# Kernel tuning notes

Measured on AMD Instinct MI355X. Metric: run time of the kernel, lower is better.

Reference implementation:

```python
import jax, jax.numpy as jnp
import numpy as np


def setup_inputs() -> dict:
    key = jax.random.key(0)
    ks = jax.random.split(key, 8)
    T, B, O, H, A = 512, 256, 720, 128, 2
    s = lambda k, shp, sc: (jax.random.normal(k, shp, jnp.float32) * sc)
    return {
        "x": jax.random.normal(ks[0], (T, B, O), jnp.float32),
        "h0": jnp.zeros((B, H), jnp.float32),
        "c0": jnp.zeros((B, H), jnp.float32),
        "Wx": s(ks[1], (O, 4 * H), 1.0 / np.sqrt(O)),
        "Wh": s(ks[2], (H, 4 * H), 1.0 / np.sqrt(H)),
        "b": jnp.zeros((4 * H,), jnp.float32),
        "Wa1": s(ks[3], (H, H), np.sqrt(2.0 / H)),
        "ba1": jnp.zeros((H,), jnp.float32),
        "Wa2": s(ks[4], (H, A), 0.01),
        "ba2": jnp.zeros((A,), jnp.float32),
        "log_std": jnp.zeros((A,), jnp.float32),
        "Wc1": s(ks[5], (H, H), np.sqrt(2.0 / H)),
        "bc1": jnp.zeros((H,), jnp.float32),
        "Wc2": s(ks[6], (H, 1), 0.01),
        "bc2": jnp.zeros((1,), jnp.float32),
    }


def _lstm(x, h0, c0, Wx, Wh, b):
    # Precompute input projections for all timesteps: [T, B, 4H]
    xW = jnp.einsum('tbo,og->tbg', x, Wx) + b

    def step(carry, xw_t):
        h, c = carry
        gates = xw_t + h @ Wh  # [B, 4H]
        i, f, g, o = jnp.split(gates, 4, axis=-1)
        c = jax.nn.sigmoid(f) * c + jax.nn.sigmoid(i) * jnp.tanh(g)
        h = jax.nn.sigmoid(o) * jnp.tanh(c)
        return (h, c), h

    (hT, cT), _ = jax.lax.scan(step, (h0, c0), xW)
    return hT, cT


def reference(x, h0, c0, Wx, Wh, b, Wa1, ba1, Wa2, ba2, log_std,
              Wc1, bc1, Wc2, bc2):
    hT, cT = _lstm(x, h0, c0, Wx, Wh, b)
    feat = hT  # outputs[-1] == last hidden state (unidirectional)
    actor_mean = jnp.tanh(feat @ Wa1 + ba1) @ Wa2 + ba2  # [B, A]
    std = jnp.exp(log_std)  # [A]
    value = (jnp.tanh(feat @ Wc1 + bc1) @ Wc2 + bc2).squeeze(-1)  # [B]
    return actor_mean, std, value, hT, cT
```

## Files before the change

### kernel.cpp

```cpp
#include <hip/hip_runtime.h>
#include <hip/hip_bf16.h>

typedef unsigned int   u32;
typedef unsigned short u16;
typedef _Float16       f16;
typedef __attribute__((ext_vector_type(2))) _Float16 f16x2;
typedef __attribute__((ext_vector_type(8))) _Float16 f16x8;
typedef __attribute__((ext_vector_type(4))) float    f32x4;
typedef __attribute__((ext_vector_type(4))) u32      u32x4;

#define T_STEPS 512
#define BATCH   256
#define O_IN    720
#define KPAD    736
#define HID     128
#define G4      512
#define OUT_STD 512
#define OUT_VAL 514
#define OUT_HT  770
#define OUT_CT  33538

static const unsigned long long XW_OFF  = 0ull;
static const unsigned long long WXT_OFF = 134217728ull;

__device__ inline float exp2raw(float x){
  float r; asm("v_exp_f32 %0, %1" : "=v"(r) : "v"(x)); return r;
}
__device__ inline float rcpraw(float x){
  float r; asm("v_rcp_f32 %0, %1" : "=v"(r) : "v"(x)); return r;
}
__device__ inline float sigf(float x){ return rcpraw(1.0f + exp2raw(-1.44269504f * x)); }
__device__ inline float tanhfast(float x){
  return fmaf(2.f, rcpraw(1.0f + exp2raw(-2.88539008f * x)), -1.f);
}

__device__ inline float dot2f(u32 a, u32 b, float c){
  float d;
  asm("v_dot2_f32_f16 %0, %1, %2, %3" : "=v"(d) : "v"(a), "v"(b), "v"(c));
  return d;
}

#define DPPF(x, ctrl) \
  __uint_as_float((u32)__builtin_amdgcn_update_dpp(0, (int)__float_as_uint(x), (ctrl), 0xF, 0xF, false))

#define HQ_STRIDE 80
#define H_BYTES   (4*HQ_STRIDE)
#define HW_OFF(j) (((j)>>5)*HQ_STRIDE + ((j)&31)*2)

__global__ void k_pack_wxt(const float* __restrict__ Wx, u16* __restrict__ wxt){
  const int n = blockIdx.x;
  for (int k = threadIdx.x; k < KPAD; k += 256){
    float v = (k < O_IN) ? Wx[(size_t)k * G4 + n] : 0.f;
    wxt[(size_t)n * KPAD + k] = __builtin_bit_cast(u16, (f16)v);
  }
}

__global__ __launch_bounds__(256, 2) void k_gemm(const float* __restrict__ x,
                                                 const u16* __restrict__ wxt,
                                                 u16* __restrict__ xw)
{
  const int l  = threadIdx.x & 63;
  const int w  = threadIdx.x >> 6;
  const int lr = l & 15;
  const int lk = l >> 4;
  const u32 L  = (blockIdx.x & 7u) * 256u + (blockIdx.x >> 3);
  const u32 mb = L >> 2, nb = L & 3u;
  const u32 M0 = mb * 256u + (u32)w * 64u;
  const u32 N0 = nb * 128u;

  const float* ax[4];
  const u16*   bx[8];
#pragma unroll
  for (int mf = 0; mf < 4; ++mf)
    ax[mf] = x + (unsigned long long)(M0 + mf*16 + lr) * O_IN + lk*8;
#pragma unroll
  for (int nf = 0; nf < 8; ++nf)
    bx[nf] = wxt + (unsigned long long)(N0 + nf*16 + lr) * KPAD + lk*8;

  f32x4 acc[4][8];
#pragma unroll
  for (int mf = 0; mf < 4; ++mf)
#pragma unroll
    for (int nf = 0; nf < 8; ++nf)
      acc[mf][nf] = (f32x4){0.f, 0.f, 0.f, 0.f};

  f32x4 a0[4][2];
  f16x8 aF[4], bF[8];

#pragma unroll
  for (int mf = 0; mf < 4; ++mf){
    a0[mf][0] = *(const f32x4*)(ax[mf]);
    a0[mf][1] = *(const f32x4*)(ax[mf] + 4);
  }
#pragma unroll
  for (int nf = 0; nf < 8; ++nf)
    bF[nf] = *(const f16x8*)(bx[nf]);
#pragma unroll
  for (int mf = 0; mf < 4; ++mf){
    f32x4 lo = a0[mf][0], hi = a0[mf][1];
    f16x8 v; v[0]=(f16)lo.x; v[1]=(f16)lo.y; v[2]=(f16)lo.z; v[3]=(f16)lo.w;
             v[4]=(f16)hi.x; v[5]=(f16)hi.y; v[6]=(f16)hi.z; v[7]=(f16)hi.w;
    aF[mf] = v;
  }

  for (int kc = 0; kc < 22; ++kc){
    if (kc < 21){
#pragma unroll
      for (int mf = 0; mf < 4; ++mf){
        a0[mf][0] = *(const f32x4*)(ax[mf] + (kc+1)*32);
        a0[mf][1] = *(const f32x4*)(ax[mf] + (kc+1)*32 + 4);
      }
    }
#pragma unroll
    for (int nf = 0; nf < 8; ++nf){
#pragma unroll
      for (int mf = 0; mf < 4; ++mf)
        acc[mf][nf] = __builtin_amdgcn_mfma_f32_16x16x32_f16(aF[mf], bF[nf], acc[mf][nf], 0, 0, 0);
      if (kc < 21)
        bF[nf] = *(const f16x8*)(bx[nf] + (kc+1)*32);
    }
    if (kc < 21){
#pragma unroll
      for (int mf = 0; mf < 4; ++mf){
        f32x4 lo = a0[mf][0], hi = a0[mf][1];
        f16x8 v; v[0]=(f16)lo.x; v[1]=(f16)lo.y; v[2]=(f16)lo.z; v[3]=(f16)lo.w;
                 v[4]=(f16)hi.x; v[5]=(f16)hi.y; v[6]=(f16)hi.z; v[7]=(f16)hi.w;
        aF[mf] = v;
      }
    }
  }

  {
    f16x8 aT[4];
#pragma unroll
    for (int mf = 0; mf < 4; ++mf) aT[mf] = (f16x8)(f16)0.f;
    if (lk < 2){
#pragma unroll
      for (int mf = 0; mf < 4; ++mf){
        f32x4 lo = *(const f32x4*)(ax[mf] + 704);
        f32x4 hi = *(const f32x4*)(ax[mf] + 708);
        f16x8 v; v[0]=(f16)lo.x; v[1]=(f16)lo.y; v[2]=(f16)lo.z; v[3]=(f16)lo.w;
                 v[4]=(f16)hi.x; v[5]=(f16)hi.y; v[6]=(f16)hi.z; v[7]=(f16)hi.w;
        aT[mf] = v;
      }
    }
#pragma unroll
    for (int nf = 0; nf < 8; ++nf){
      f16x8 bT = *(const f16x8*)(bx[nf] + 704);
#pragma unroll
      for (int mf = 0; mf < 4; ++mf)
        acc[mf][nf] = __builtin_amdgcn_mfma_f32_16x16x32_f16(aT[mf], bT, acc[mf][nf], 0, 0, 0);
    }
  }

#pragma unroll
  for (int mf = 0; mf < 4; ++mf){
    const u32 rowb = M0 + mf*16 + lk*4;
#pragma unroll
    for (int nf = 0; nf < 8; ++nf){
      const u32 col = N0 + nf*16 + lr;
#pragma unroll
      for (int r = 0; r < 4; ++r)
        xw[(unsigned long long)(rowb + r) * G4 + col] = __builtin_bit_cast(u16, (f16)acc[mf][nf][r]);
    }
  }
}

__global__ __attribute__((amdgpu_flat_work_group_size(512,512), amdgpu_waves_per_eu(2,2)))
void k_rnn(
    const u16* __restrict__ xw, const float* __restrict__ Wh,
    const float* __restrict__ h0, const float* __restrict__ c0,
    const float* __restrict__ bvec,
    const float* __restrict__ Wa1, const float* __restrict__ ba1,
    const float* __restrict__ Wa2, const float* __restrict__ ba2,
    const float* __restrict__ Wc1, const float* __restrict__ bc1,
    const float* __restrict__ Wc2, const float* __restrict__ bc2,
    const float* __restrict__ log_std, float* __restrict__ out)
{
  const int b = blockIdx.x;
  const int t = threadIdx.x;
  const int j = t >> 2;
  const int q = t & 3;

  __shared__ __align__(16) char hbuf[2][H_BYTES];
  __shared__ __align__(16) float hf[HID];
  __shared__ float hid[256];

  u32 wg0[16], wg1[16], wg2[16], wg3[16];
#pragma unroll
  for (int m = 0; m < 16; ++m){
    const u32 kb = (u32)(32*q + 2*m) * G4 + (u32)j;
    f16x2 p;
    p[0]=(f16)Wh[kb      ]; p[1]=(f16)Wh[kb+G4      ]; wg0[m]=__builtin_bit_cast(u32,p);
    p[0]=(f16)Wh[kb+128  ]; p[1]=(f16)Wh[kb+G4+128  ]; wg1[m]=__builtin_bit_cast(u32,p);
    p[0]=(f16)Wh[kb+256  ]; p[1]=(f16)Wh[kb+G4+256  ]; wg2[m]=__builtin_bit_cast(u32,p);
    p[0]=(f16)Wh[kb+384  ]; p[1]=(f16)Wh[kb+G4+384  ]; wg3[m]=__builtin_bit_cast(u32,p);
  }
#pragma unroll
  for (int m = 0; m < 16; ++m){
    asm volatile("" : "+v"(wg0[m]));
    asm volatile("" : "+v"(wg1[m]));
    asm volatile("" : "+v"(wg2[m]));
    asm volatile("" : "+v"(wg3[m]));
  }
  const float bb = bvec[j + 128*q];

  const float kexp  = (q == 2) ? -2.88539008f : -1.44269504f;
  const float postm = (q == 2) ? 2.f : 1.f;
  const float posta = (q == 2) ? -1.f : 0.f;

  float cs = c0[b*HID + j];
  float hv = h0[b*HID + j];
  if (q == 0)
    *(u16*)(hbuf[0] + HW_OFF(j)) = __builtin_bit_cast(u16, (f16)hv);
  __syncthreads();

  const u16* xp = xw + (u32)b * G4 + (u32)(j + 128*q);
  float xc  = (float)__builtin_bit_cast(f16, xp[0]) + bb;
  float xn1 = (T_STEPS > 1) ? (float)__builtin_bit_cast(f16, xp[131072u]) + bb : 0.f;

  for (int s = 0; s < T_STEPS; ++s){
    const char* hq = hbuf[s & 1] + q * HQ_STRIDE;

    float xn2 = 0.f;
    if (s + 2 < T_STEPS)
      xn2 = (float)__builtin_bit_cast(f16, xp[(u32)(s+2) * 131072u]) + bb;

    float p0 = 0.f, p1 = 0.f, p2 = 0.f, p3 = 0.f;
#pragma unroll
    for (int it = 0; it < 4; ++it){
      u32x4 hh = *(const u32x4*)(hq + it*16);
#pragma unroll
      for (int z = 0; z < 4; ++z){
        p0 = dot2f(hh[z], wg0[4*it+z], p0);
        p1 = dot2f(hh[z], wg1[4*it+z], p1);
        p2 = dot2f(hh[z], wg2[4*it+z], p2);
        p3 = dot2f(hh[z], wg3[4*it+z], p3);
      }
    }
    p0 += DPPF(p0, 177);  p1 += DPPF(p1, 177);
    p2 += DPPF(p2, 177);  p3 += DPPF(p3, 177);
    p0 += DPPF(p0, 78);   p1 += DPPF(p1, 78);
    p2 += DPPF(p2, 78);   p3 += DPPF(p3, 78);

    float gsum = (q == 0) ? p0 : (q == 1) ? p1 : (q == 2) ? p2 : p3;
    float gval = gsum + xc;
    float r    = rcpraw(1.0f + exp2raw(kexp * gval));
    float av   = fmaf(postm, r, posta);

    float ai = DPPF(av, 0);
    float af = DPPF(av, 85);
    float ag = DPPF(av, 170);
    float ao = DPPF(av, 255);

    cs = af * cs + ai * ag;
    hv = ao * tanhfast(cs);
    if (q == 0)
      *(u16*)(hbuf[(s & 1) ^ 1] + HW_OFF(j)) = __builtin_bit_cast(u16, (f16)hv);
    __syncthreads();
    xc = xn1; xn1 = xn2;
  }

  if (q == 0){
    out[OUT_HT + b*HID + j] = hv;
    out[OUT_CT + b*HID + j] = cs;
    hf[j] = hv;
  }
  __syncthreads();

  if (t < 256){
    const float* W = (t < HID) ? Wa1 : Wc1;
    const int col  = t & (HID - 1);
    const f32x4* hp4 = (const f32x4*)hf;
    float a0 = 0.f, a1 = 0.f, a2 = 0.f, a3 = 0.f;
#pragma unroll
    for (int qq = 0; qq < 32; ++qq){
      f32x4 hh = hp4[qq];
      a0 = fmaf(hh.x, W[(u32)(4*qq+0)*HID + col], a0);
      a1 = fmaf(hh.y, W[(u32)(4*qq+1)*HID + col], a1);
      a2 = fmaf(hh.z, W[(u32)(4*qq+2)*HID + col], a2);
      a3 = fmaf(hh.w, W[(u32)(4*qq+3)*HID + col], a3);
    }
    float a = (a0 + a1) + (a2 + a3);
    hid[t] = (t < HID) ? tanhfast(a + ba1[col]) : tanhfast(a + bc1[col]);
  }
  __syncthreads();

  {
    const int wv = t >> 6, lane = t & 63;
    float p = 0.f;
    if (wv == 0)      p = hid[lane]     * Wa2[lane*2]   + hid[lane+64]     * Wa2[(lane+64)*2];
    else if (wv == 1) p = hid[lane]     * Wa2[lane*2+1] + hid[lane+64]     * Wa2[(lane+64)*2+1];
    else if (wv == 2) p = hid[128+lane] * Wc2[lane]     + hid[128+lane+64] * Wc2[lane+64];
#pragma unroll
    for (int off = 32; off > 0; off >>= 1) p += __shfl_down(p, off);
    if (lane == 0){
      if (wv == 0) out[b*2 + 0]   = p + ba2[0];
      if (wv == 1) out[b*2 + 1]   = p + ba2[1];
      if (wv == 2) out[OUT_VAL+b] = p + bc2[0];
    }
    if (b == 0 && wv == 3 && lane < 2) out[OUT_STD + lane] = expf(log_std[lane]);
  }
}

extern "C" void kernel_launch(void* const* d_in, const int* in_sizes, int n_in,
                              void* d_out, int out_size, void* d_ws, size_t ws_size,
                              hipStream_t stream)
{
  (void)in_sizes; (void)n_in; (void)out_size; (void)ws_size;
  const float* x    = (const float*)d_in[0];
  const float* h0   = (const float*)d_in[1];
  const float* c0   = (const float*)d_in[2];
  const float* Wx   = (const float*)d_in[3];
  const float* Wh   = (const float*)d_in[4];
  const float* bv   = (const float*)d_in[5];
  const float* Wa1  = (const float*)d_in[6];
  const float* ba1  = (const float*)d_in[7];
  const float* Wa2  = (const float*)d_in[8];
  const float* ba2  = (const float*)d_in[9];
  const float* lstd = (const float*)d_in[10];
  const float* Wc1  = (const float*)d_in[11];
  const float* bc1  = (const float*)d_in[12];
  const float* Wc2  = (const float*)d_in[13];
  const float* bc2  = (const float*)d_in[14];
  float* out = (float*)d_out;
  char*  ws  = (char*)d_ws;

  u16* xw  = (u16*)(ws + XW_OFF);
  u16* wxt = (u16*)(ws + WXT_OFF);

  k_pack_wxt<<<dim3(512),  dim3(256), 0, stream>>>(Wx, wxt);
  k_gemm<<<dim3(2048),     dim3(256), 0, stream>>>(x, wxt, xw);
  k_rnn<<<dim3(256),       dim3(512), 0, stream>>>(xw, Wh, h0, c0, bv,
                                                   Wa1, ba1, Wa2, ba2, Wc1, bc1, Wc2, bc2,
                                                   lstd, out);
}
```

Baseline: 722.8 us.

## Split LSTM recurrence across 1024 threads with single h buffer and shuffles

The recurrent kernel now uses 1024 threads per batch row: each thread handles one gate of one hidden unit over half of the K dimension. Each thread therefore holds 32 weight registers instead of 64 and runs a shorter dot-product chain. Gate exchange moves from DPP to ds_bpermute-style shuffles, and the double-buffered h is replaced by a single buffer. That buffer needs two barriers per step, adding sync cost and shuffle latency on the serial critical path.

```diff
diff --git a/kernel.cpp b/kernel.cpp
--- a/kernel.cpp
+++ b/kernel.cpp
@@ -29,7 +29,6 @@
 __device__ inline float rcpraw(float x){
   float r; asm("v_rcp_f32 %0, %1" : "=v"(r) : "v"(x)); return r;
 }
-__device__ inline float sigf(float x){ return rcpraw(1.0f + exp2raw(-1.44269504f * x)); }
 __device__ inline float tanhfast(float x){
   return fmaf(2.f, rcpraw(1.0f + exp2raw(-2.88539008f * x)), -1.f);
 }
@@ -40,12 +39,9 @@
   return d;
 }
 
-#define DPPF(x, ctrl) \
-  __uint_as_float((u32)__builtin_amdgcn_update_dpp(0, (int)__float_as_uint(x), (ctrl), 0xF, 0xF, false))
-
-#define HQ_STRIDE 80
-#define H_BYTES   (4*HQ_STRIDE)
-#define HW_OFF(j) (((j)>>5)*HQ_STRIDE + ((j)&31)*2)
+#define HH_STRIDE 144
+#define H_BYTES   (2*HH_STRIDE)
+#define HW_OFF(j) (((j)>>6)*HH_STRIDE + ((j)&63)*2)
 
 __global__ void k_pack_wxt(const float* __restrict__ Wx, u16* __restrict__ wxt){
   const int n = blockIdx.x;
@@ -166,7 +162,7 @@
   }
 }
 
-__global__ __attribute__((amdgpu_flat_work_group_size(512,512), amdgpu_waves_per_eu(2,2)))
+__global__ __attribute__((amdgpu_flat_work_group_size(1024,1024), amdgpu_waves_per_eu(4,4)))
 void k_rnn(
     const u16* __restrict__ xw, const float* __restrict__ Wh,
     const float* __restrict__ h0, const float* __restrict__ c0,
@@ -179,48 +175,43 @@
 {
   const int b = blockIdx.x;
   const int t = threadIdx.x;
-  const int j = t >> 2;
-  const int q = t & 3;
-
-  __shared__ __align__(16) char hbuf[2][H_BYTES];
+  const int j = t >> 3;
+  const int g = (t >> 1) & 3;
+  const int q = t & 1;
+  const int l = t & 63;
+  const int lb = l & 56;
+
+  __shared__ __align__(16) char hbuf[H_BYTES];
   __shared__ __align__(16) float hf[HID];
   __shared__ float hid[256];
 
-  u32 wg0[16], wg1[16], wg2[16], wg3[16];
-#pragma unroll
-  for (int m = 0; m < 16; ++m){
-    const u32 kb = (u32)(32*q + 2*m) * G4 + (u32)j;
-    f16x2 p;
-    p[0]=(f16)Wh[kb      ]; p[1]=(f16)Wh[kb+G4      ]; wg0[m]=__builtin_bit_cast(u32,p);
-    p[0]=(f16)Wh[kb+128  ]; p[1]=(f16)Wh[kb+G4+128  ]; wg1[m]=__builtin_bit_cast(u32,p);
-    p[0]=(f16)Wh[kb+256  ]; p[1]=(f16)Wh[kb+G4+256  ]; wg2[m]=__builtin_bit_cast(u32,p);
-    p[0]=(f16)Wh[kb+384  ]; p[1]=(f16)Wh[kb+G4+384  ]; wg3[m]=__builtin_bit_cast(u32,p);
-  }
-#pragma unroll
-  for (int m = 0; m < 16; ++m){
-    asm volatile("" : "+v"(wg0[m]));
-    asm volatile("" : "+v"(wg1[m]));
-    asm volatile("" : "+v"(wg2[m]));
-    asm volatile("" : "+v"(wg3[m]));
-  }
-  const float bb = bvec[j + 128*q];
-
-  const float kexp  = (q == 2) ? -2.88539008f : -1.44269504f;
-  const float postm = (q == 2) ? 2.f : 1.f;
-  const float posta = (q == 2) ? -1.f : 0.f;
+  u32 wg[32];
+#pragma unroll
+  for (int m = 0; m < 32; ++m){
+    const u32 kb = (u32)(64*q + 2*m) * G4 + (u32)(j + 128*g);
+    f16x2 p; p[0] = (f16)Wh[kb]; p[1] = (f16)Wh[kb + G4];
+    wg[m] = __builtin_bit_cast(u32, p);
+  }
+#pragma unroll
+  for (int m = 0; m < 32; ++m) asm volatile("" : "+v"(wg[m]));
+
+  const float bb = bvec[j + 128*g];
+  const float kexp  = (g == 2) ? -2.88539008f : -1.44269504f;
+  const float postm = (g == 2) ? 2.f : 1.f;
+  const float posta = (g == 2) ? -1.f : 0.f;
 
   float cs = c0[b*HID + j];
   float hv = h0[b*HID + j];
-  if (q == 0)
-    *(u16*)(hbuf[0] + HW_OFF(j)) = __builtin_bit_cast(u16, (f16)hv);
+  if ((t & 7) == 0)
+    *(u16*)(hbuf + HW_OFF(j)) = __builtin_bit_cast(u16, (f16)hv);
   __syncthreads();
 
-  const u16* xp = xw + (u32)b * G4 + (u32)(j + 128*q);
+  const u16* xp = xw + (u32)b * G4 + (u32)(j + 128*g);
   float xc  = (float)__builtin_bit_cast(f16, xp[0]) + bb;
   float xn1 = (T_STEPS > 1) ? (float)__builtin_bit_cast(f16, xp[131072u]) + bb : 0.f;
 
   for (int s = 0; s < T_STEPS; ++s){
-    const char* hq = hbuf[s & 1] + q * HQ_STRIDE;
+    const char* hq = hbuf + q * HH_STRIDE;
 
     float xn2 = 0.f;
     if (s + 2 < T_STEPS)
@@ -228,40 +219,35 @@
 
     float p0 = 0.f, p1 = 0.f, p2 = 0.f, p3 = 0.f;
 #pragma unroll
-    for (int it = 0; it < 4; ++it){
+    for (int it = 0; it < 8; ++it){
       u32x4 hh = *(const u32x4*)(hq + it*16);
-#pragma unroll
-      for (int z = 0; z < 4; ++z){
-        p0 = dot2f(hh[z], wg0[4*it+z], p0);
-        p1 = dot2f(hh[z], wg1[4*it+z], p1);
-        p2 = dot2f(hh[z], wg2[4*it+z], p2);
-        p3 = dot2f(hh[z], wg3[4*it+z], p3);
-      }
-    }
-    p0 += DPPF(p0, 177);  p1 += DPPF(p1, 177);
-    p2 += DPPF(p2, 177);  p3 += DPPF(p3, 177);
-    p0 += DPPF(p0, 78);   p1 += DPPF(p1, 78);
-    p2 += DPPF(p2, 78);   p3 += DPPF(p3, 78);
-
-    float gsum = (q == 0) ? p0 : (q == 1) ? p1 : (q == 2) ? p2 : p3;
-    float gval = gsum + xc;
-    float r    = rcpraw(1.0f + exp2raw(kexp * gval));
-    float av   = fmaf(postm, r, posta);
-
-    float ai = DPPF(av, 0);
-    float af = DPPF(av, 85);
-    float ag = DPPF(av, 170);
-    float ao = DPPF(av, 255);
+      p0 = dot2f(hh.x, wg[4*it+0], p0);
+      p1 = dot2f(hh.y, wg[4*it+1], p1);
+      p2 = dot2f(hh.z, wg[4*it+2], p2);
+      p3 = dot2f(hh.w, wg[4*it+3], p3);
+    }
+    float p = (p0 + p1) + (p2 + p3);
+    p += __shfl_xor(p, 1);
+
+    float gval = p + xc;
+    float av   = fmaf(postm, rcpraw(1.0f + exp2raw(kexp * gval)), posta);
+
+    float ai = __shfl(av, lb | 0);
+    float af = __shfl(av, lb | 2);
+    float ag = __shfl(av, lb | 4);
+    float ao = __shfl(av, lb | 6);
 
     cs = af * cs + ai * ag;
     hv = ao * tanhfast(cs);
-    if (q == 0)
-      *(u16*)(hbuf[(s & 1) ^ 1] + HW_OFF(j)) = __builtin_bit_cast(u16, (f16)hv);
+
+    __syncthreads();
+    if ((t & 7) == 0)
+      *(u16*)(hbuf + HW_OFF(j)) = __builtin_bit_cast(u16, (f16)hv);
     __syncthreads();
     xc = xn1; xn1 = xn2;
   }
 
-  if (q == 0){
+  if ((t & 7) == 0){
     out[OUT_HT + b*HID + j] = hv;
     out[OUT_CT + b*HID + j] = cs;
     hf[j] = hv;
@@ -292,12 +278,14 @@
     if (wv == 0)      p = hid[lane]     * Wa2[lane*2]   + hid[lane+64]     * Wa2[(lane+64)*2];
     else if (wv == 1) p = hid[lane]     * Wa2[lane*2+1] + hid[lane+64]     * Wa2[(lane+64)*2+1];
     else if (wv == 2) p = hid[128+lane] * Wc2[lane]     + hid[128+lane+64] * Wc2[lane+64];
-#pragma unroll
-    for (int off = 32; off > 0; off >>= 1) p += __shfl_down(p, off);
-    if (lane == 0){
-      if (wv == 0) out[b*2 + 0]   = p + ba2[0];
-      if (wv == 1) out[b*2 + 1]   = p + ba2[1];
-      if (wv == 2) out[OUT_VAL+b] = p + bc2[0];
+    if (wv < 3){
+#pragma unroll
+      for (int off = 32; off > 0; off >>= 1) p += __shfl_down(p, off);
+      if (lane == 0){
+        if (wv == 0) out[b*2 + 0]   = p + ba2[0];
+        if (wv == 1) out[b*2 + 1]   = p + ba2[1];
+        if (wv == 2) out[OUT_VAL+b] = p + bc2[0];
+      }
     }
     if (b == 0 && wv == 3 && lane < 2) out[OUT_STD + lane] = expf(log_std[lane]);
   }
@@ -329,9 +317,9 @@
   u16* xw  = (u16*)(ws + XW_OFF);
   u16* wxt = (u16*)(ws + WXT_OFF);
 
-  k_pack_wxt<<<dim3(512),  dim3(256), 0, stream>>>(Wx, wxt);
-  k_gemm<<<dim3(2048),     dim3(256), 0, stream>>>(x, wxt, xw);
-  k_rnn<<<dim3(256),       dim3(512), 0, stream>>>(xw, Wh, h0, c0, bv,
-                                                   Wa1, ba1, Wa2, ba2, Wc1, bc1, Wc2, bc2,
-                                                   lstd, out);
-}
+  k_pack_wxt<<<dim3(512),  dim3(256),  0, stream>>>(Wx, wxt);
+  k_gemm<<<dim3(2048),     dim3(256),  0, stream>>>(x, wxt, xw);
+  k_rnn<<<dim3(256),       dim3(1024), 0, stream>>>(xw, Wh, h0, c0, bv,
+                                                    Wa1, ba1, Wa2, ba2, Wc1, bc1, Wc2, bc2,
+                                                    lstd, out);
+}
```

Measured after the change: 865.5 us. 19.7% more time.
